# Kernel tuning notes

Measured on AMD Instinct MI355X. Metric: run time of the kernel, lower is better.

The kernel has to match this reference:

```python
import jax, jax.numpy as jnp
import numpy as np

GROUP_SIZE = 128
QMAX = 127.0  # int8 symmetric: 2^(8-1) - 1
EPS = 1e-8


def group_quant_dequant(t, group_size=GROUP_SIZE):
    """Group-wise symmetric int8 fake-quantize along the last dim.

    Groups of `group_size` along the last axis share one scale
    s = max|t| / 127; values are rounded/clipped to int8 range and
    immediately dequantized (q * s), which is the exact math of a
    group-quantized GEMM with inline dequantization.
    """
    shape = t.shape
    g = t.reshape(shape[:-1] + (shape[-1] // group_size, group_size))
    s = jnp.maximum(jnp.max(jnp.abs(g), axis=-1, keepdims=True) / QMAX, EPS)
    q = jnp.clip(jnp.round(g / s), -QMAX, QMAX)
    return (q * s).reshape(shape)


def setup_inputs() -> dict:
    key = jax.random.key(0)
    k0, k1, k2, k3 = jax.random.split(key, 4)
    B, S, H, I = 2, 2048, 4096, 11008
    x = jax.random.normal(k0, (B, S, H), dtype=jnp.float32)
    # Linear weights stored [out_features, in_features]; quant groups run
    # along the in_features (contraction) axis.
    w_gate = jax.random.normal(k1, (I, H), dtype=jnp.float32) * (1.0 / np.sqrt(H))
    w_up = jax.random.normal(k2, (I, H), dtype=jnp.float32) * (1.0 / np.sqrt(H))
    w_down = jax.random.normal(k3, (H, I), dtype=jnp.float32) * (1.0 / np.sqrt(I))
    return {"x": x, "w_gate": w_gate, "w_up": w_up, "w_down": w_down}


def reference(x, w_gate, w_up, w_down):
    # quantize input activations (QuantTensor(x))
    xq = group_quant_dequant(x)
    # gate/up quant-GEMMs with inline weight dequant
    gate = jnp.einsum('bsh,ih->bsi', xq, group_quant_dequant(w_gate))
    up = jnp.einsum('bsh,ih->bsi', xq, group_quant_dequant(w_up))
    # SwiGLU: SiLU(gate) * up, then requantize the hidden activation
    hidden = jax.nn.silu(gate) * up
    hq = group_quant_dequant(hidden)
    # down quant-GEMM -> dequantized float output
    out = jnp.einsum('bsi,hi->bsh', hq, group_quant_dequant(w_down))
    return out
```

## Files before the change

kernel.cpp:

```cpp
#include <hip/hip_runtime.h>
#include <math.h>

typedef int i32x4 __attribute__((ext_vector_type(4)));
typedef float f32x4 __attribute__((ext_vector_type(4)));
typedef float f32x2 __attribute__((ext_vector_type(2)));

#define QMAXF 127.0f
#define EPSQ 1e-8f

__device__ __forceinline__ void gl_lds16(const void* g, void* l) {
  __builtin_amdgcn_global_load_lds(
      (const __attribute__((address_space(1))) unsigned int*)g,
      (__attribute__((address_space(3))) unsigned int*)l, 16, 0, 0);
}
__device__ __forceinline__ void gl_lds4(const void* g, void* l) {
  __builtin_amdgcn_global_load_lds(
      (const __attribute__((address_space(1))) unsigned int*)g,
      (__attribute__((address_space(3))) unsigned int*)l, 4, 0, 0);
}

__global__ __launch_bounds__(256)
void qdq8(const float* __restrict__ in, char* __restrict__ q,
          float* __restrict__ sT, long n_groups, int gpr, int R) {
  long wid = (long)blockIdx.x * 4 + (threadIdx.x >> 6);
  if (wid >= n_groups) return;
  int lane = threadIdx.x & 63;
  long base = wid * 128 + lane * 2;
  f32x2 v = *(const f32x2*)(in + base);
  float m = fmaxf(fabsf(v.x), fabsf(v.y));
#pragma unroll
  for (int off = 32; off; off >>= 1) m = fmaxf(m, __shfl_xor(m, off));
  float s = fmaxf(m / QMAXF, EPSQ);
  int q0 = (int)fminf(fmaxf(rintf(v.x / s), -QMAXF), QMAXF);
  int q1 = (int)fminf(fmaxf(rintf(v.y / s), -QMAXF), QMAXF);
  *(unsigned short*)(q + base) =
      (unsigned short)((q0 & 0xff) | ((q1 & 0xff) << 8));
  if (lane == 0) {
    long row = wid / gpr;
    long gc = wid - row * gpr;
    sT[gc * (long)R + row] = s;
  }
}


__global__ __launch_bounds__(256) __attribute__((amdgpu_waves_per_eu(2, 2)))
void gemm_gu_i8(const char* __restrict__ Aq, const char* __restrict__ Bg,
                const char* __restrict__ Bu,
                const float* __restrict__ sAT, const float* __restrict__ sGT,
                const float* __restrict__ sUT,
                char* __restrict__ Hq, float* __restrict__ sHT,
                int M, int N, int K, int NBN) {
  __shared__ char sA[16384];
  __shared__ char sBG[16384];
  __shared__ char sBU[16384];
  __shared__ float sSa[128], sSg[128], sSu[128];
  __shared__ float rmx[2][128];
  __shared__ float rs[128];

  const int tid = threadIdx.x;
  const int lane = tid & 63;
  const int wid = tid >> 6;
  const int wr = (wid >> 1) * 64;
  const int wc = (wid & 1) * 64;
  const int l15 = lane & 15, l16 = lane >> 4;

  const int nwg = gridDim.x;
  const int wg = ((int)blockIdx.x & 7) * (nwg >> 3) + ((int)blockIdx.x >> 3);
  const long m0 = (long)(wg / NBN) * 128;
  const long n0 = (long)(wg % NBN) * 128;

  const char* gA[4];
  const char* gG[4];
  const char* gU[4];
#pragma unroll
  for (int k = 0; k < 4; k++) {
    int c = tid + 256 * k;
    long row = c >> 3;
    int off = ((c & 7) * 16) ^ ((int)(row & 7) << 4);
    gA[k] = Aq + (m0 + row) * K + off;
    gG[k] = Bg + (n0 + row) * K + off;
    gU[k] = Bu + (n0 + row) * K + off;
  }

  const int rdSwz = (l15 & 7) << 4;
  const int colK0 = (l16 * 16) ^ rdSwz;
  const int colK1 = (64 + l16 * 16) ^ rdSwz;

  f32x4 accg[4][4], accu[4][4];
#pragma unroll
  for (int i = 0; i < 4; i++)
#pragma unroll
    for (int j = 0; j < 4; j++) {
      accg[i][j] = (f32x4){0.f, 0.f, 0.f, 0.f};
      accu[i][j] = (f32x4){0.f, 0.f, 0.f, 0.f};
    }
  const i32x4 iz = {0, 0, 0, 0};

  const int KG = K >> 7;
  for (int g = 0; g < KG; ++g) {
    const long kb = (long)g << 7;
#pragma unroll
    for (int k = 0; k < 4; k++) {
      gl_lds16(gA[k] + kb, &sA[(tid + 256 * k) * 16]);
      gl_lds16(gG[k] + kb, &sBG[(tid + 256 * k) * 16]);
      gl_lds16(gU[k] + kb, &sBU[(tid + 256 * k) * 16]);
    }
    if (wid < 2) {
      gl_lds4(sAT + (long)g * M + m0 + tid, &sSa[wid * 64]);
      gl_lds4(sUT + (long)g * N + n0 + tid, &sSu[wid * 64]);
    } else {
      gl_lds4(sGT + (long)g * N + n0 + (tid - 128), &sSg[(wid - 2) * 64]);
    }
    __syncthreads();

    i32x4 af[4][2];
#pragma unroll
    for (int i = 0; i < 4; i++) {
      const int rb = (wr + i * 16 + l15) * 128;
      af[i][0] = *(const i32x4*)&sA[rb + colK0];
      af[i][1] = *(const i32x4*)&sA[rb + colK1];
    }
    f32x4 sa4[4];
#pragma unroll
    for (int i = 0; i < 4; i++)
      sa4[i] = *(const f32x4*)&sSa[wr + i * 16 + l16 * 4];

#pragma unroll
    for (int j = 0; j < 4; j++) {
      const int rbB = (wc + j * 16 + l15) * 128;
      i32x4 bgf[2], buf_[2];
      bgf[0] = *(const i32x4*)&sBG[rbB + colK0];
      bgf[1] = *(const i32x4*)&sBG[rbB + colK1];
      buf_[0] = *(const i32x4*)&sBU[rbB + colK0];
      buf_[1] = *(const i32x4*)&sBU[rbB + colK1];
      float sbg = sSg[wc + j * 16 + l15];
      float sbu = sSu[wc + j * 16 + l15];
#pragma unroll
      for (int i = 0; i < 4; i++) {
        i32x4 tg = __builtin_amdgcn_mfma_i32_16x16x64_i8(af[i][0], bgf[0], iz, 0, 0, 0);
        tg = __builtin_amdgcn_mfma_i32_16x16x64_i8(af[i][1], bgf[1], tg, 0, 0, 0);
        i32x4 tu = __builtin_amdgcn_mfma_i32_16x16x64_i8(af[i][0], buf_[0], iz, 0, 0, 0);
        tu = __builtin_amdgcn_mfma_i32_16x16x64_i8(af[i][1], buf_[1], tu, 0, 0, 0);
        f32x4 mg = sa4[i] * sbg;
        f32x4 mu = sa4[i] * sbu;
        accg[i][j] += mg * __builtin_convertvector(tg, f32x4);
        accu[i][j] += mu * __builtin_convertvector(tu, f32x4);
      }
    }
    __syncthreads();
  }

  float pm[4][4];
#pragma unroll
  for (int i = 0; i < 4; i++)
#pragma unroll
    for (int r = 0; r < 4; r++) pm[i][r] = 0.f;
#pragma unroll
  for (int i = 0; i < 4; i++)
#pragma unroll
    for (int j = 0; j < 4; j++)
#pragma unroll
      for (int r = 0; r < 4; r++) {
        float gv = accg[i][j][r];
        float h = gv / (1.f + expf(-gv)) * accu[i][j][r];
        accu[i][j][r] = h;
        pm[i][r] = fmaxf(pm[i][r], fabsf(h));
      }
#pragma unroll
  for (int i = 0; i < 4; i++)
#pragma unroll
    for (int r = 0; r < 4; r++) {
      pm[i][r] = fmaxf(pm[i][r], __shfl_xor(pm[i][r], 1));
      pm[i][r] = fmaxf(pm[i][r], __shfl_xor(pm[i][r], 2));
      pm[i][r] = fmaxf(pm[i][r], __shfl_xor(pm[i][r], 4));
      pm[i][r] = fmaxf(pm[i][r], __shfl_xor(pm[i][r], 8));
    }
#pragma unroll
  for (int i = 0; i < 4; i++)
#pragma unroll
    for (int r = 0; r < 4; r++)
      if (l15 == i * 4 + r) rmx[wid & 1][wr + i * 16 + l16 * 4 + r] = pm[i][r];
  __syncthreads();
  if (tid < 128) {
    float mx = fmaxf(rmx[0][tid], rmx[1][tid]);
    float s = fmaxf(mx / QMAXF, EPSQ);
    rs[tid] = s;
    sHT[(n0 >> 7) * (long)M + m0 + tid] = s;
  }
  __syncthreads();
#pragma unroll
  for (int i = 0; i < 4; i++) {
    f32x4 sr = *(const f32x4*)&rs[wr + i * 16 + l16 * 4];
#pragma unroll
    for (int j = 0; j < 4; j++)
#pragma unroll
      for (int r = 0; r < 4; r++) {
        float qv = fminf(fmaxf(rintf(accu[i][j][r] / sr[r]), -QMAXF), QMAXF);
        sA[(wr + i * 16 + l16 * 4 + r) * 128 + wc + j * 16 + l15] = (char)(int)qv;
      }
  }
  __syncthreads();
  {
    int row = tid >> 1, seg = tid & 1;
    const i32x4* src = (const i32x4*)&sA[row * 128 + seg * 64];
    i32x4* dst = (i32x4*)(Hq + (m0 + row) * N + n0 + seg * 64);
#pragma unroll
    for (int k = 0; k < 4; k++) dst[k] = src[k];
  }
}

__global__ __launch_bounds__(256) __attribute__((amdgpu_waves_per_eu(2, 2)))
void gemm_dn_i8(const char* __restrict__ Aq, const char* __restrict__ Bq,
                const float* __restrict__ sAT, const float* __restrict__ sBT,
                float* __restrict__ C, int M, int N, int K, int NBN) {
  __shared__ char sA[16384];
  __shared__ char sB[16384];
  __shared__ float sSa[128], sSb[128];

  const int tid = threadIdx.x;
  const int lane = tid & 63;
  const int wid = tid >> 6;
  const int wr = (wid >> 1) * 64;
  const int wc = (wid & 1) * 64;
  const int l15 = lane & 15, l16 = lane >> 4;

  const int nwg = gridDim.x;
  const int wg = ((int)blockIdx.x & 7) * (nwg >> 3) + ((int)blockIdx.x >> 3);
  const long m0 = (long)(wg / NBN) * 128;
  const long n0 = (long)(wg % NBN) * 128;

  const char* gA[4];
  const char* gB[4];
#pragma unroll
  for (int k = 0; k < 4; k++) {
    int c = tid + 256 * k;
    long row = c >> 3;
    int off = ((c & 7) * 16) ^ ((int)(row & 7) << 4);
    gA[k] = Aq + (m0 + row) * K + off;
    gB[k] = Bq + (n0 + row) * K + off;
  }

  const int rdSwz = (l15 & 7) << 4;
  const int colK0 = (l16 * 16) ^ rdSwz;
  const int colK1 = (64 + l16 * 16) ^ rdSwz;

  f32x4 acc[4][4];
#pragma unroll
  for (int i = 0; i < 4; i++)
#pragma unroll
    for (int j = 0; j < 4; j++) acc[i][j] = (f32x4){0.f, 0.f, 0.f, 0.f};
  const i32x4 iz = {0, 0, 0, 0};

  const int KG = K >> 7;
  for (int g = 0; g < KG; ++g) {
    const long kb = (long)g << 7;
#pragma unroll
    for (int k = 0; k < 4; k++) {
      gl_lds16(gA[k] + kb, &sA[(tid + 256 * k) * 16]);
      gl_lds16(gB[k] + kb, &sB[(tid + 256 * k) * 16]);
    }
    if (wid < 2) {
      gl_lds4(sAT + (long)g * M + m0 + tid, &sSa[wid * 64]);
    } else {
      gl_lds4(sBT + (long)g * N + n0 + (tid - 128), &sSb[(wid - 2) * 64]);
    }
    __syncthreads();

    i32x4 af[4][2];
#pragma unroll
    for (int i = 0; i < 4; i++) {
      const int rb = (wr + i * 16 + l15) * 128;
      af[i][0] = *(const i32x4*)&sA[rb + colK0];
      af[i][1] = *(const i32x4*)&sA[rb + colK1];
    }
    f32x4 sa4[4];
#pragma unroll
    for (int i = 0; i < 4; i++)
      sa4[i] = *(const f32x4*)&sSa[wr + i * 16 + l16 * 4];

#pragma unroll
    for (int j = 0; j < 4; j++) {
      const int rbB = (wc + j * 16 + l15) * 128;
      i32x4 bf[2];
      bf[0] = *(const i32x4*)&sB[rbB + colK0];
      bf[1] = *(const i32x4*)&sB[rbB + colK1];
      float sb = sSb[wc + j * 16 + l15];
#pragma unroll
      for (int i = 0; i < 4; i++) {
        i32x4 t = __builtin_amdgcn_mfma_i32_16x16x64_i8(af[i][0], bf[0], iz, 0, 0, 0);
        t = __builtin_amdgcn_mfma_i32_16x16x64_i8(af[i][1], bf[1], t, 0, 0, 0);
        f32x4 ms = sa4[i] * sb;
        acc[i][j] += ms * __builtin_convertvector(t, f32x4);
      }
    }
    __syncthreads();
  }

#pragma unroll
  for (int i = 0; i < 4; i++)
#pragma unroll
    for (int j = 0; j < 4; j++)
#pragma unroll
      for (int r = 0; r < 4; r++) {
        long row = m0 + wr + i * 16 + l16 * 4 + r;
        long col = n0 + wc + j * 16 + l15;
        C[row * N + col] = acc[i][j][r];
      }
}

extern "C" void kernel_launch(void* const* d_in, const int* in_sizes, int n_in,
                              void* d_out, int out_size, void* d_ws, size_t ws_size,
                              hipStream_t stream) {
  (void)n_in; (void)out_size;
  const float* x  = (const float*)d_in[0];
  const float* wg = (const float*)d_in[1];
  const float* wu = (const float*)d_in[2];
  const float* wd = (const float*)d_in[3];
  float* out = (float*)d_out;

  const long H = 4096;
  const long M = in_sizes[0] / H;
  const long I = in_sizes[1] / H;
  const long GH = H >> 7;
  const long GI = I >> 7;

  char* ws = (char*)d_ws;
  size_t off = 0;
  char* xq  = ws + off; off += (size_t)(M * H);
  char* wgq = ws + off; off += (size_t)(I * H);
  char* wuq = ws + off; off += (size_t)(I * H);
  char* wdq = ws + off; off += (size_t)(H * I);
  char* hq  = ws + off; off += (size_t)(M * I);
  float* s_x = (float*)(ws + off); off += (size_t)(GH * M) * 4;
  float* s_g = (float*)(ws + off); off += (size_t)(GH * I) * 4;
  float* s_u = (float*)(ws + off); off += (size_t)(GH * I) * 4;
  float* s_d = (float*)(ws + off); off += (size_t)(GI * H) * 4;
  float* s_h = (float*)(ws + off); off += (size_t)(GI * M) * 4;
  if (ws_size < off) return;

  {
    long ng;
    ng = M * H / 128;
    qdq8<<<dim3((unsigned)((ng + 3) / 4)), dim3(256), 0, stream>>>(x, xq, s_x, ng, (int)GH, (int)M);
    ng = I * H / 128;
    qdq8<<<dim3((unsigned)((ng + 3) / 4)), dim3(256), 0, stream>>>(wg, wgq, s_g, ng, (int)GH, (int)I);
    qdq8<<<dim3((unsigned)((ng + 3) / 4)), dim3(256), 0, stream>>>(wu, wuq, s_u, ng, (int)GH, (int)I);
    ng = H * I / 128;
    qdq8<<<dim3((unsigned)((ng + 3) / 4)), dim3(256), 0, stream>>>(wd, wdq, s_d, ng, (int)GI, (int)H);
  }

  {
    const int NBN = (int)GI;
    const int grid = (int)(M / 128) * NBN;
    gemm_gu_i8<<<dim3(grid), dim3(256), 0, stream>>>(
        xq, wgq, wuq, s_x, s_g, s_u, hq, s_h, (int)M, (int)I, (int)H, NBN);
  }
  {
    const int NBN = (int)GH;
    const int grid = (int)(M / 128) * NBN;
    gemm_dn_i8<<<dim3(grid), dim3(256), 0, stream>>>(
        hq, wdq, s_h, s_d, out, (int)M, (int)H, (int)I, NBN);
  }
}
```

Measured before the change: 1.168 ms.

## Double-buffer LDS and enlarge GEMM tiles to 256x128 with 512 threads

Both int8 GEMM kernels switch from static 48KB/32KB shared buffers to dynamic LDS holding two stages. The next K-group's operand and scale tiles are loaded asynchronously (global_load_lds) while the current group is computed, which removes one barrier per iteration. The block tile grows from 128x128 to 256x128 with 8 waves, which halves the grid and increases reuse of the B/weight tiles. The large LDS footprint (~135KB and ~99KB) likely limits each CU to one block. That trades occupancy-based latency hiding for explicit prefetching.

```diff
diff --git a/kernel.cpp b/kernel.cpp
--- a/kernel.cpp
+++ b/kernel.cpp
@@ -43,44 +43,37 @@
 }
 
 
-__global__ __launch_bounds__(256) __attribute__((amdgpu_waves_per_eu(2, 2)))
+#define GU_SC 131072
+#define GU_RMX 135168
+#define GU_RS 137216
+#define GU_LDS 138240
+
+__global__ __launch_bounds__(512, 2)
 void gemm_gu_i8(const char* __restrict__ Aq, const char* __restrict__ Bg,
                 const char* __restrict__ Bu,
                 const float* __restrict__ sAT, const float* __restrict__ sGT,
                 const float* __restrict__ sUT,
                 char* __restrict__ Hq, float* __restrict__ sHT,
                 int M, int N, int K, int NBN) {
-  __shared__ char sA[16384];
-  __shared__ char sBG[16384];
-  __shared__ char sBU[16384];
-  __shared__ float sSa[128], sSg[128], sSu[128];
-  __shared__ float rmx[2][128];
-  __shared__ float rs[128];
-
+  extern __shared__ __align__(16) char smem[];
   const int tid = threadIdx.x;
   const int lane = tid & 63;
   const int wid = tid >> 6;
-  const int wr = (wid >> 1) * 64;
-  const int wc = (wid & 1) * 64;
+  const int wm = wid >> 1, wn = wid & 1;
+  const int wr = wm * 64, wc = wn * 64;
   const int l15 = lane & 15, l16 = lane >> 4;
 
   const int nwg = gridDim.x;
   const int wg = ((int)blockIdx.x & 7) * (nwg >> 3) + ((int)blockIdx.x >> 3);
-  const long m0 = (long)(wg / NBN) * 128;
+  const long m0 = (long)(wg / NBN) * 256;
   const long n0 = (long)(wg % NBN) * 128;
 
-  const char* gA[4];
-  const char* gG[4];
-  const char* gU[4];
-#pragma unroll
-  for (int k = 0; k < 4; k++) {
-    int c = tid + 256 * k;
-    long row = c >> 3;
-    int off = ((c & 7) * 16) ^ ((int)(row & 7) << 4);
-    gA[k] = Aq + (m0 + row) * K + off;
-    gG[k] = Bg + (n0 + row) * K + off;
-    gU[k] = Bu + (n0 + row) * K + off;
-  }
+  const long rowS = tid >> 3;
+  const int offS = ((tid & 7) * 16) ^ ((int)(rowS & 7) << 4);
+  const long kstr = 64L * K;
+  const char* gA0 = Aq + (m0 + rowS) * K + offS;
+  const char* gG0 = Bg + (n0 + rowS) * K + offS;
+  const char* gU0 = Bu + (n0 + rowS) * K + offS;
 
   const int rdSwz = (l15 & 7) << 4;
   const int colK0 = (l16 * 16) ^ rdSwz;
@@ -95,46 +88,60 @@
       accu[i][j] = (f32x4){0.f, 0.f, 0.f, 0.f};
     }
   const i32x4 iz = {0, 0, 0, 0};
-
   const int KG = K >> 7;
+
+#define GU_STAGE(gg, bb)                                                      \
+  {                                                                           \
+    const long kb = (long)(gg) << 7;                                          \
+    char* tb = smem + (bb) * 65536;                                           \
+    _Pragma("unroll") for (int k = 0; k < 4; k++)                             \
+        gl_lds16(gA0 + kb + k * kstr, tb + (tid + 512 * k) * 16);             \
+    _Pragma("unroll") for (int k = 0; k < 2; k++) {                           \
+      gl_lds16(gG0 + kb + k * kstr, tb + 32768 + (tid + 512 * k) * 16);       \
+      gl_lds16(gU0 + kb + k * kstr, tb + 49152 + (tid + 512 * k) * 16);       \
+    }                                                                         \
+    char* sc = smem + GU_SC + (bb) * 2048;                                    \
+    if (wid < 4) {                                                            \
+      gl_lds4(sAT + (long)(gg) * M + m0 + tid, sc + wid * 256);               \
+    } else if (wid < 6) {                                                     \
+      gl_lds4(sGT + (long)(gg) * N + n0 + (tid - 256), sc + 1024 + (wid - 4) * 256); \
+    } else {                                                                  \
+      gl_lds4(sUT + (long)(gg) * N + n0 + (tid - 384), sc + 1536 + (wid - 6) * 256); \
+    }                                                                         \
+  }
+
+  GU_STAGE(0, 0);
+  __syncthreads();
+
   for (int g = 0; g < KG; ++g) {
-    const long kb = (long)g << 7;
-#pragma unroll
-    for (int k = 0; k < 4; k++) {
-      gl_lds16(gA[k] + kb, &sA[(tid + 256 * k) * 16]);
-      gl_lds16(gG[k] + kb, &sBG[(tid + 256 * k) * 16]);
-      gl_lds16(gU[k] + kb, &sBU[(tid + 256 * k) * 16]);
-    }
-    if (wid < 2) {
-      gl_lds4(sAT + (long)g * M + m0 + tid, &sSa[wid * 64]);
-      gl_lds4(sUT + (long)g * N + n0 + tid, &sSu[wid * 64]);
-    } else {
-      gl_lds4(sGT + (long)g * N + n0 + (tid - 128), &sSg[(wid - 2) * 64]);
-    }
-    __syncthreads();
+    const int cb = g & 1;
+    if (g + 1 < KG) GU_STAGE(g + 1, cb ^ 1);
+
+    const char* tb = smem + cb * 65536;
+    const float* sc = (const float*)(smem + GU_SC + cb * 2048);
 
     i32x4 af[4][2];
 #pragma unroll
     for (int i = 0; i < 4; i++) {
       const int rb = (wr + i * 16 + l15) * 128;
-      af[i][0] = *(const i32x4*)&sA[rb + colK0];
-      af[i][1] = *(const i32x4*)&sA[rb + colK1];
+      af[i][0] = *(const i32x4*)(tb + rb + colK0);
+      af[i][1] = *(const i32x4*)(tb + rb + colK1);
     }
     f32x4 sa4[4];
 #pragma unroll
     for (int i = 0; i < 4; i++)
-      sa4[i] = *(const f32x4*)&sSa[wr + i * 16 + l16 * 4];
+      sa4[i] = *(const f32x4*)(sc + wr + i * 16 + l16 * 4);
 
 #pragma unroll
     for (int j = 0; j < 4; j++) {
       const int rbB = (wc + j * 16 + l15) * 128;
       i32x4 bgf[2], buf_[2];
-      bgf[0] = *(const i32x4*)&sBG[rbB + colK0];
-      bgf[1] = *(const i32x4*)&sBG[rbB + colK1];
-      buf_[0] = *(const i32x4*)&sBU[rbB + colK0];
-      buf_[1] = *(const i32x4*)&sBU[rbB + colK1];
-      float sbg = sSg[wc + j * 16 + l15];
-      float sbu = sSu[wc + j * 16 + l15];
+      bgf[0] = *(const i32x4*)(tb + 32768 + rbB + colK0);
+      bgf[1] = *(const i32x4*)(tb + 32768 + rbB + colK1);
+      buf_[0] = *(const i32x4*)(tb + 49152 + rbB + colK0);
+      buf_[1] = *(const i32x4*)(tb + 49152 + rbB + colK1);
+      float sbg = sc[256 + wc + j * 16 + l15];
+      float sbu = sc[384 + wc + j * 16 + l15];
 #pragma unroll
       for (int i = 0; i < 4; i++) {
         i32x4 tg = __builtin_amdgcn_mfma_i32_16x16x64_i8(af[i][0], bgf[0], iz, 0, 0, 0);
@@ -150,6 +157,8 @@
     __syncthreads();
   }
 
+  float* rmx = (float*)(smem + GU_RMX);
+  float* rs = (float*)(smem + GU_RS);
   float pm[4][4];
 #pragma unroll
   for (int i = 0; i < 4; i++)
@@ -179,66 +188,62 @@
   for (int i = 0; i < 4; i++)
 #pragma unroll
     for (int r = 0; r < 4; r++)
-      if (l15 == i * 4 + r) rmx[wid & 1][wr + i * 16 + l16 * 4 + r] = pm[i][r];
-  __syncthreads();
-  if (tid < 128) {
-    float mx = fmaxf(rmx[0][tid], rmx[1][tid]);
+      if (l15 == i * 4 + r) rmx[wn * 256 + wr + i * 16 + l16 * 4 + r] = pm[i][r];
+  __syncthreads();
+  if (tid < 256) {
+    float mx = fmaxf(rmx[tid], rmx[256 + tid]);
     float s = fmaxf(mx / QMAXF, EPSQ);
     rs[tid] = s;
     sHT[(n0 >> 7) * (long)M + m0 + tid] = s;
   }
   __syncthreads();
+  char* sQ = smem;
 #pragma unroll
   for (int i = 0; i < 4; i++) {
-    f32x4 sr = *(const f32x4*)&rs[wr + i * 16 + l16 * 4];
+    f32x4 sr = *(const f32x4*)(rs + wr + i * 16 + l16 * 4);
 #pragma unroll
     for (int j = 0; j < 4; j++)
 #pragma unroll
       for (int r = 0; r < 4; r++) {
         float qv = fminf(fmaxf(rintf(accu[i][j][r] / sr[r]), -QMAXF), QMAXF);
-        sA[(wr + i * 16 + l16 * 4 + r) * 128 + wc + j * 16 + l15] = (char)(int)qv;
+        sQ[(wr + i * 16 + l16 * 4 + r) * 128 + wc + j * 16 + l15] = (char)(int)qv;
       }
   }
   __syncthreads();
   {
     int row = tid >> 1, seg = tid & 1;
-    const i32x4* src = (const i32x4*)&sA[row * 128 + seg * 64];
+    const i32x4* src = (const i32x4*)(sQ + row * 128 + seg * 64);
     i32x4* dst = (i32x4*)(Hq + (m0 + row) * N + n0 + seg * 64);
 #pragma unroll
     for (int k = 0; k < 4; k++) dst[k] = src[k];
   }
 }
 
-__global__ __launch_bounds__(256) __attribute__((amdgpu_waves_per_eu(2, 2)))
+#define DN_SC 98304
+#define DN_LDS 101376
+
+__global__ __launch_bounds__(512, 2)
 void gemm_dn_i8(const char* __restrict__ Aq, const char* __restrict__ Bq,
                 const float* __restrict__ sAT, const float* __restrict__ sBT,
                 float* __restrict__ C, int M, int N, int K, int NBN) {
-  __shared__ char sA[16384];
-  __shared__ char sB[16384];
-  __shared__ float sSa[128], sSb[128];
-
+  extern __shared__ __align__(16) char smem[];
   const int tid = threadIdx.x;
   const int lane = tid & 63;
   const int wid = tid >> 6;
-  const int wr = (wid >> 1) * 64;
-  const int wc = (wid & 1) * 64;
+  const int wm = wid >> 1, wn = wid & 1;
+  const int wr = wm * 64, wc = wn * 64;
   const int l15 = lane & 15, l16 = lane >> 4;
 
   const int nwg = gridDim.x;
   const int wg = ((int)blockIdx.x & 7) * (nwg >> 3) + ((int)blockIdx.x >> 3);
-  const long m0 = (long)(wg / NBN) * 128;
+  const long m0 = (long)(wg / NBN) * 256;
   const long n0 = (long)(wg % NBN) * 128;
 
-  const char* gA[4];
-  const char* gB[4];
-#pragma unroll
-  for (int k = 0; k < 4; k++) {
-    int c = tid + 256 * k;
-    long row = c >> 3;
-    int off = ((c & 7) * 16) ^ ((int)(row & 7) << 4);
-    gA[k] = Aq + (m0 + row) * K + off;
-    gB[k] = Bq + (n0 + row) * K + off;
-  }
+  const long rowS = tid >> 3;
+  const int offS = ((tid & 7) * 16) ^ ((int)(rowS & 7) << 4);
+  const long kstr = 64L * K;
+  const char* gA0 = Aq + (m0 + rowS) * K + offS;
+  const char* gB0 = Bq + (n0 + rowS) * K + offS;
 
   const int rdSwz = (l15 & 7) << 4;
   const int colK0 = (l16 * 16) ^ rdSwz;
@@ -250,41 +255,53 @@
 #pragma unroll
     for (int j = 0; j < 4; j++) acc[i][j] = (f32x4){0.f, 0.f, 0.f, 0.f};
   const i32x4 iz = {0, 0, 0, 0};
-
   const int KG = K >> 7;
+
+#define DN_STAGE(gg, bb)                                                      \
+  {                                                                           \
+    const long kb = (long)(gg) << 7;                                          \
+    char* tb = smem + (bb) * 49152;                                           \
+    _Pragma("unroll") for (int k = 0; k < 4; k++)                             \
+        gl_lds16(gA0 + kb + k * kstr, tb + (tid + 512 * k) * 16);             \
+    _Pragma("unroll") for (int k = 0; k < 2; k++)                             \
+        gl_lds16(gB0 + kb + k * kstr, tb + 32768 + (tid + 512 * k) * 16);     \
+    char* sc = smem + DN_SC + (bb) * 1536;                                    \
+    if (wid < 4) {                                                            \
+      gl_lds4(sAT + (long)(gg) * M + m0 + tid, sc + wid * 256);               \
+    } else if (wid < 6) {                                                     \
+      gl_lds4(sBT + (long)(gg) * N + n0 + (tid - 256), sc + 1024 + (wid - 4) * 256); \
+    }                                                                         \
+  }
+
+  DN_STAGE(0, 0);
+  __syncthreads();
+
   for (int g = 0; g < KG; ++g) {
-    const long kb = (long)g << 7;
-#pragma unroll
-    for (int k = 0; k < 4; k++) {
-      gl_lds16(gA[k] + kb, &sA[(tid + 256 * k) * 16]);
-      gl_lds16(gB[k] + kb, &sB[(tid + 256 * k) * 16]);
-    }
-    if (wid < 2) {
-      gl_lds4(sAT + (long)g * M + m0 + tid, &sSa[wid * 64]);
-    } else {
-      gl_lds4(sBT + (long)g * N + n0 + (tid - 128), &sSb[(wid - 2) * 64]);
-    }
-    __syncthreads();
+    const int cb = g & 1;
+    if (g + 1 < KG) DN_STAGE(g + 1, cb ^ 1);
+
+    const char* tb = smem + cb * 49152;
+    const float* sc = (const float*)(smem + DN_SC + cb * 1536);
 
     i32x4 af[4][2];
 #pragma unroll
     for (int i = 0; i < 4; i++) {
       const int rb = (wr + i * 16 + l15) * 128;
-      af[i][0] = *(const i32x4*)&sA[rb + colK0];
-      af[i][1] = *(const i32x4*)&sA[rb + colK1];
+      af[i][0] = *(const i32x4*)(tb + rb + colK0);
+      af[i][1] = *(const i32x4*)(tb + rb + colK1);
     }
     f32x4 sa4[4];
 #pragma unroll
     for (int i = 0; i < 4; i++)
-      sa4[i] = *(const f32x4*)&sSa[wr + i * 16 + l16 * 4];
+      sa4[i] = *(const f32x4*)(sc + wr + i * 16 + l16 * 4);
 
 #pragma unroll
     for (int j = 0; j < 4; j++) {
       const int rbB = (wc + j * 16 + l15) * 128;
       i32x4 bf[2];
-      bf[0] = *(const i32x4*)&sB[rbB + colK0];
-      bf[1] = *(const i32x4*)&sB[rbB + colK1];
-      float sb = sSb[wc + j * 16 + l15];
+      bf[0] = *(const i32x4*)(tb + 32768 + rbB + colK0);
+      bf[1] = *(const i32x4*)(tb + 32768 + rbB + colK1);
+      float sb = sc[256 + wc + j * 16 + l15];
 #pragma unroll
       for (int i = 0; i < 4; i++) {
         i32x4 t = __builtin_amdgcn_mfma_i32_16x16x64_i8(af[i][0], bf[0], iz, 0, 0, 0);
@@ -338,6 +355,11 @@
   float* s_h = (float*)(ws + off); off += (size_t)(GI * M) * 4;
   if (ws_size < off) return;
 
+  hipFuncSetAttribute((const void*)gemm_gu_i8,
+                      hipFuncAttributeMaxDynamicSharedMemorySize, GU_LDS);
+  hipFuncSetAttribute((const void*)gemm_dn_i8,
+                      hipFuncAttributeMaxDynamicSharedMemorySize, DN_LDS);
+
   {
     long ng;
     ng = M * H / 128;
@@ -351,14 +373,14 @@
 
   {
     const int NBN = (int)GI;
-    const int grid = (int)(M / 128) * NBN;
-    gemm_gu_i8<<<dim3(grid), dim3(256), 0, stream>>>(
+    const int grid = (int)(M / 256) * NBN;
+    gemm_gu_i8<<<dim3(grid), dim3(512), GU_LDS, stream>>>(
         xq, wgq, wuq, s_x, s_g, s_u, hq, s_h, (int)M, (int)I, (int)H, NBN);
   }
   {
     const int NBN = (int)GH;
-    const int grid = (int)(M / 128) * NBN;
-    gemm_dn_i8<<<dim3(grid), dim3(256), 0, stream>>>(
+    const int grid = (int)(M / 256) * NBN;
+    gemm_dn_i8<<<dim3(grid), dim3(512), DN_LDS, stream>>>(
         hq, wdq, s_h, s_d, out, (int)M, (int)H, (int)I, NBN);
   }
 }
```

Result: faster. 1.117 ms (-4.4%).

## Shrink GEMM tiles to 64x128 with 512-thread blocks and 8 waves

Applied to the files above, without the earlier changes.

Both int8 GEMM kernels move from 128x128 tiles with 4 waves (64x64 per wave) to 64x128 tiles with 8 waves (32x32 per wave) and 512 threads per block. The launch grid doubles. This raises wave count and occupancy and lowers register pressure per wave. In exchange, each MFMA gets less operand reuse and global traffic per output rises, because the B tile is reloaded twice as often across M.

```diff
diff --git a/kernel.cpp b/kernel.cpp
--- a/kernel.cpp
+++ b/kernel.cpp
@@ -43,90 +43,83 @@
 }
 
 
-__global__ __launch_bounds__(256) __attribute__((amdgpu_waves_per_eu(2, 2)))
+__global__ __launch_bounds__(512, 4)
 void gemm_gu_i8(const char* __restrict__ Aq, const char* __restrict__ Bg,
                 const char* __restrict__ Bu,
                 const float* __restrict__ sAT, const float* __restrict__ sGT,
                 const float* __restrict__ sUT,
                 char* __restrict__ Hq, float* __restrict__ sHT,
                 int M, int N, int K, int NBN) {
-  __shared__ char sA[16384];
-  __shared__ char sBG[16384];
-  __shared__ char sBU[16384];
-  __shared__ float sSa[128], sSg[128], sSu[128];
-  __shared__ float rmx[2][128];
-  __shared__ float rs[128];
+  __shared__ __align__(16) char sA[8192];
+  __shared__ __align__(16) char sBG[16384];
+  __shared__ __align__(16) char sBU[16384];
+  __shared__ float sSa[64], sSg[128], sSu[128];
+  __shared__ float rmx[4][64];
+  __shared__ float rs[64];
 
   const int tid = threadIdx.x;
   const int lane = tid & 63;
   const int wid = tid >> 6;
-  const int wr = (wid >> 1) * 64;
-  const int wc = (wid & 1) * 64;
+  const int wm = wid >> 2, wn = wid & 3;
+  const int wr = wm * 32, wc = wn * 32;
   const int l15 = lane & 15, l16 = lane >> 4;
 
   const int nwg = gridDim.x;
   const int wg = ((int)blockIdx.x & 7) * (nwg >> 3) + ((int)blockIdx.x >> 3);
-  const long m0 = (long)(wg / NBN) * 128;
+  const long m0 = (long)(wg / NBN) * 64;
   const long n0 = (long)(wg % NBN) * 128;
 
-  const char* gA[4];
-  const char* gG[4];
-  const char* gU[4];
-#pragma unroll
-  for (int k = 0; k < 4; k++) {
-    int c = tid + 256 * k;
-    long row = c >> 3;
-    int off = ((c & 7) * 16) ^ ((int)(row & 7) << 4);
-    gA[k] = Aq + (m0 + row) * K + off;
-    gG[k] = Bg + (n0 + row) * K + off;
-    gU[k] = Bu + (n0 + row) * K + off;
-  }
+  const long rowS = tid >> 3;
+  const int offS = ((tid & 7) * 16) ^ ((int)(rowS & 7) << 4);
+  const long kstr = 64L * K;
+  const char* gA0 = Aq + (m0 + rowS) * K + offS;
+  const char* gG0 = Bg + (n0 + rowS) * K + offS;
+  const char* gU0 = Bu + (n0 + rowS) * K + offS;
 
   const int rdSwz = (l15 & 7) << 4;
   const int colK0 = (l16 * 16) ^ rdSwz;
   const int colK1 = (64 + l16 * 16) ^ rdSwz;
 
-  f32x4 accg[4][4], accu[4][4];
-#pragma unroll
-  for (int i = 0; i < 4; i++)
-#pragma unroll
-    for (int j = 0; j < 4; j++) {
+  f32x4 accg[2][2], accu[2][2];
+#pragma unroll
+  for (int i = 0; i < 2; i++)
+#pragma unroll
+    for (int j = 0; j < 2; j++) {
       accg[i][j] = (f32x4){0.f, 0.f, 0.f, 0.f};
       accu[i][j] = (f32x4){0.f, 0.f, 0.f, 0.f};
     }
   const i32x4 iz = {0, 0, 0, 0};
-
   const int KG = K >> 7;
+
   for (int g = 0; g < KG; ++g) {
     const long kb = (long)g << 7;
-#pragma unroll
-    for (int k = 0; k < 4; k++) {
-      gl_lds16(gA[k] + kb, &sA[(tid + 256 * k) * 16]);
-      gl_lds16(gG[k] + kb, &sBG[(tid + 256 * k) * 16]);
-      gl_lds16(gU[k] + kb, &sBU[(tid + 256 * k) * 16]);
-    }
-    if (wid < 2) {
-      gl_lds4(sAT + (long)g * M + m0 + tid, &sSa[wid * 64]);
-      gl_lds4(sUT + (long)g * N + n0 + tid, &sSu[wid * 64]);
-    } else {
-      gl_lds4(sGT + (long)g * N + n0 + (tid - 128), &sSg[(wid - 2) * 64]);
-    }
+    gl_lds16(gA0 + kb, &sA[tid * 16]);
+#pragma unroll
+    for (int k = 0; k < 2; k++) {
+      gl_lds16(gG0 + kb + k * kstr, &sBG[(tid + 512 * k) * 16]);
+      gl_lds16(gU0 + kb + k * kstr, &sBU[(tid + 512 * k) * 16]);
+    }
+    if (wid == 0) gl_lds4(sAT + (long)g * M + m0 + lane, &sSa[0]);
+    else if (wid == 1) gl_lds4(sGT + (long)g * N + n0 + lane, &sSg[0]);
+    else if (wid == 2) gl_lds4(sGT + (long)g * N + n0 + 64 + lane, &sSg[64]);
+    else if (wid == 3) gl_lds4(sUT + (long)g * N + n0 + lane, &sSu[0]);
+    else if (wid == 4) gl_lds4(sUT + (long)g * N + n0 + 64 + lane, &sSu[64]);
     __syncthreads();
 
-    i32x4 af[4][2];
-#pragma unroll
-    for (int i = 0; i < 4; i++) {
+    i32x4 af[2][2];
+#pragma unroll
+    for (int i = 0; i < 2; i++) {
       const int rb = (wr + i * 16 + l15) * 128;
       af[i][0] = *(const i32x4*)&sA[rb + colK0];
       af[i][1] = *(const i32x4*)&sA[rb + colK1];
     }
-    f32x4 sa4[4];
-#pragma unroll
-    for (int i = 0; i < 4; i++)
+    f32x4 sa4[2];
+#pragma unroll
+    for (int i = 0; i < 2; i++)
       sa4[i] = *(const f32x4*)&sSa[wr + i * 16 + l16 * 4];
 
 #pragma unroll
-    for (int j = 0; j < 4; j++) {
+    for (int j = 0; j < 2; j++) {
       const int rbB = (wc + j * 16 + l15) * 128;
       i32x4 bgf[2], buf_[2];
       bgf[0] = *(const i32x4*)&sBG[rbB + colK0];
@@ -136,29 +129,27 @@
       float sbg = sSg[wc + j * 16 + l15];
       float sbu = sSu[wc + j * 16 + l15];
 #pragma unroll
-      for (int i = 0; i < 4; i++) {
+      for (int i = 0; i < 2; i++) {
         i32x4 tg = __builtin_amdgcn_mfma_i32_16x16x64_i8(af[i][0], bgf[0], iz, 0, 0, 0);
         tg = __builtin_amdgcn_mfma_i32_16x16x64_i8(af[i][1], bgf[1], tg, 0, 0, 0);
         i32x4 tu = __builtin_amdgcn_mfma_i32_16x16x64_i8(af[i][0], buf_[0], iz, 0, 0, 0);
         tu = __builtin_amdgcn_mfma_i32_16x16x64_i8(af[i][1], buf_[1], tu, 0, 0, 0);
-        f32x4 mg = sa4[i] * sbg;
-        f32x4 mu = sa4[i] * sbu;
-        accg[i][j] += mg * __builtin_convertvector(tg, f32x4);
-        accu[i][j] += mu * __builtin_convertvector(tu, f32x4);
+        accg[i][j] += (sa4[i] * sbg) * __builtin_convertvector(tg, f32x4);
+        accu[i][j] += (sa4[i] * sbu) * __builtin_convertvector(tu, f32x4);
       }
     }
     __syncthreads();
   }
 
-  float pm[4][4];
-#pragma unroll
-  for (int i = 0; i < 4; i++)
+  float pm[2][4];
+#pragma unroll
+  for (int i = 0; i < 2; i++)
 #pragma unroll
     for (int r = 0; r < 4; r++) pm[i][r] = 0.f;
 #pragma unroll
-  for (int i = 0; i < 4; i++)
-#pragma unroll
-    for (int j = 0; j < 4; j++)
+  for (int i = 0; i < 2; i++)
+#pragma unroll
+    for (int j = 0; j < 2; j++)
 #pragma unroll
       for (int r = 0; r < 4; r++) {
         float gv = accg[i][j][r];
@@ -167,7 +158,7 @@
         pm[i][r] = fmaxf(pm[i][r], fabsf(h));
       }
 #pragma unroll
-  for (int i = 0; i < 4; i++)
+  for (int i = 0; i < 2; i++)
 #pragma unroll
     for (int r = 0; r < 4; r++) {
       pm[i][r] = fmaxf(pm[i][r], __shfl_xor(pm[i][r], 1));
@@ -176,23 +167,24 @@
       pm[i][r] = fmaxf(pm[i][r], __shfl_xor(pm[i][r], 8));
     }
 #pragma unroll
-  for (int i = 0; i < 4; i++)
+  for (int i = 0; i < 2; i++)
 #pragma unroll
     for (int r = 0; r < 4; r++)
-      if (l15 == i * 4 + r) rmx[wid & 1][wr + i * 16 + l16 * 4 + r] = pm[i][r];
+      if (l15 == i * 4 + r) rmx[wn][wr + i * 16 + l16 * 4 + r] = pm[i][r];
   __syncthreads();
-  if (tid < 128) {
-    float mx = fmaxf(rmx[0][tid], rmx[1][tid]);
+  if (tid < 64) {
+    float mx = fmaxf(fmaxf(rmx[0][tid], rmx[1][tid]),
+                     fmaxf(rmx[2][tid], rmx[3][tid]));
     float s = fmaxf(mx / QMAXF, EPSQ);
     rs[tid] = s;
     sHT[(n0 >> 7) * (long)M + m0 + tid] = s;
   }
   __syncthreads();
 #pragma unroll
-  for (int i = 0; i < 4; i++) {
+  for (int i = 0; i < 2; i++) {
     f32x4 sr = *(const f32x4*)&rs[wr + i * 16 + l16 * 4];
 #pragma unroll
-    for (int j = 0; j < 4; j++)
+    for (int j = 0; j < 2; j++)
 #pragma unroll
       for (int r = 0; r < 4; r++) {
         float qv = fminf(fmaxf(rintf(accu[i][j][r] / sr[r]), -QMAXF), QMAXF);
@@ -201,105 +193,94 @@
   }
   __syncthreads();
   {
-    int row = tid >> 1, seg = tid & 1;
-    const i32x4* src = (const i32x4*)&sA[row * 128 + seg * 64];
-    i32x4* dst = (i32x4*)(Hq + (m0 + row) * N + n0 + seg * 64);
-#pragma unroll
-    for (int k = 0; k < 4; k++) dst[k] = src[k];
-  }
-}
-
-__global__ __launch_bounds__(256) __attribute__((amdgpu_waves_per_eu(2, 2)))
+    long row = tid >> 3;
+    int off = (tid & 7) * 16;
+    *(i32x4*)(Hq + (m0 + row) * N + n0 + off) = *(const i32x4*)&sA[row * 128 + off];
+  }
+}
+
+__global__ __launch_bounds__(512, 4)
 void gemm_dn_i8(const char* __restrict__ Aq, const char* __restrict__ Bq,
                 const float* __restrict__ sAT, const float* __restrict__ sBT,
                 float* __restrict__ C, int M, int N, int K, int NBN) {
-  __shared__ char sA[16384];
-  __shared__ char sB[16384];
-  __shared__ float sSa[128], sSb[128];
+  __shared__ __align__(16) char sA[8192];
+  __shared__ __align__(16) char sB[16384];
+  __shared__ float sSa[64], sSb[128];
 
   const int tid = threadIdx.x;
   const int lane = tid & 63;
   const int wid = tid >> 6;
-  const int wr = (wid >> 1) * 64;
-  const int wc = (wid & 1) * 64;
+  const int wm = wid >> 2, wn = wid & 3;
+  const int wr = wm * 32, wc = wn * 32;
   const int l15 = lane & 15, l16 = lane >> 4;
 
   const int nwg = gridDim.x;
   const int wg = ((int)blockIdx.x & 7) * (nwg >> 3) + ((int)blockIdx.x >> 3);
-  const long m0 = (long)(wg / NBN) * 128;
+  const long m0 = (long)(wg / NBN) * 64;
   const long n0 = (long)(wg % NBN) * 128;
 
-  const char* gA[4];
-  const char* gB[4];
-#pragma unroll
-  for (int k = 0; k < 4; k++) {
-    int c = tid + 256 * k;
-    long row = c >> 3;
-    int off = ((c & 7) * 16) ^ ((int)(row & 7) << 4);
-    gA[k] = Aq + (m0 + row) * K + off;
-    gB[k] = Bq + (n0 + row) * K + off;
-  }
+  const long rowS = tid >> 3;
+  const int offS = ((tid & 7) * 16) ^ ((int)(rowS & 7) << 4);
+  const long kstr = 64L * K;
+  const char* gA0 = Aq + (m0 + rowS) * K + offS;
+  const char* gB0 = Bq + (n0 + rowS) * K + offS;
 
   const int rdSwz = (l15 & 7) << 4;
   const int colK0 = (l16 * 16) ^ rdSwz;
   const int colK1 = (64 + l16 * 16) ^ rdSwz;
 
-  f32x4 acc[4][4];
-#pragma unroll
-  for (int i = 0; i < 4; i++)
-#pragma unroll
-    for (int j = 0; j < 4; j++) acc[i][j] = (f32x4){0.f, 0.f, 0.f, 0.f};
+  f32x4 acc[2][2];
+#pragma unroll
+  for (int i = 0; i < 2; i++)
+#pragma unroll
+    for (int j = 0; j < 2; j++) acc[i][j] = (f32x4){0.f, 0.f, 0.f, 0.f};
   const i32x4 iz = {0, 0, 0, 0};
-
   const int KG = K >> 7;
+
   for (int g = 0; g < KG; ++g) {
     const long kb = (long)g << 7;
-#pragma unroll
-    for (int k = 0; k < 4; k++) {
-      gl_lds16(gA[k] + kb, &sA[(tid + 256 * k) * 16]);
-      gl_lds16(gB[k] + kb, &sB[(tid + 256 * k) * 16]);
-    }
-    if (wid < 2) {
-      gl_lds4(sAT + (long)g * M + m0 + tid, &sSa[wid * 64]);
-    } else {
-      gl_lds4(sBT + (long)g * N + n0 + (tid - 128), &sSb[(wid - 2) * 64]);
-    }
+    gl_lds16(gA0 + kb, &sA[tid * 16]);
+#pragma unroll
+    for (int k = 0; k < 2; k++)
+      gl_lds16(gB0 + kb + k * kstr, &sB[(tid + 512 * k) * 16]);
+    if (wid == 0) gl_lds4(sAT + (long)g * M + m0 + lane, &sSa[0]);
+    else if (wid == 1) gl_lds4(sBT + (long)g * N + n0 + lane, &sSb[0]);
+    else if (wid == 2) gl_lds4(sBT + (long)g * N + n0 + 64 + lane, &sSb[64]);
     __syncthreads();
 
-    i32x4 af[4][2];
-#pragma unroll
-    for (int i = 0; i < 4; i++) {
+    i32x4 af[2][2];
+#pragma unroll
+    for (int i = 0; i < 2; i++) {
       const int rb = (wr + i * 16 + l15) * 128;
       af[i][0] = *(const i32x4*)&sA[rb + colK0];
       af[i][1] = *(const i32x4*)&sA[rb + colK1];
     }
-    f32x4 sa4[4];
-#pragma unroll
-    for (int i = 0; i < 4; i++)
+    f32x4 sa4[2];
+#pragma unroll
+    for (int i = 0; i < 2; i++)
       sa4[i] = *(const f32x4*)&sSa[wr + i * 16 + l16 * 4];
 
 #pragma unroll
-    for (int j = 0; j < 4; j++) {
+    for (int j = 0; j < 2; j++) {
       const int rbB = (wc + j * 16 + l15) * 128;
       i32x4 bf[2];
       bf[0] = *(const i32x4*)&sB[rbB + colK0];
       bf[1] = *(const i32x4*)&sB[rbB + colK1];
       float sb = sSb[wc + j * 16 + l15];
 #pragma unroll
-      for (int i = 0; i < 4; i++) {
+      for (int i = 0; i < 2; i++) {
         i32x4 t = __builtin_amdgcn_mfma_i32_16x16x64_i8(af[i][0], bf[0], iz, 0, 0, 0);
         t = __builtin_amdgcn_mfma_i32_16x16x64_i8(af[i][1], bf[1], t, 0, 0, 0);
-        f32x4 ms = sa4[i] * sb;
-        acc[i][j] += ms * __builtin_convertvector(t, f32x4);
+        acc[i][j] += (sa4[i] * sb) * __builtin_convertvector(t, f32x4);
       }
     }
     __syncthreads();
   }
 
 #pragma unroll
-  for (int i = 0; i < 4; i++)
-#pragma unroll
-    for (int j = 0; j < 4; j++)
+  for (int i = 0; i < 2; i++)
+#pragma unroll
+    for (int j = 0; j < 2; j++)
 #pragma unroll
       for (int r = 0; r < 4; r++) {
         long row = m0 + wr + i * 16 + l16 * 4 + r;
@@ -351,14 +332,14 @@
 
   {
     const int NBN = (int)GI;
-    const int grid = (int)(M / 128) * NBN;
-    gemm_gu_i8<<<dim3(grid), dim3(256), 0, stream>>>(
+    const int grid = (int)(M / 64) * NBN;
+    gemm_gu_i8<<<dim3(grid), dim3(512), 0, stream>>>(
         xq, wgq, wuq, s_x, s_g, s_u, hq, s_h, (int)M, (int)I, (int)H, NBN);
   }
   {
     const int NBN = (int)GH;
-    const int grid = (int)(M / 128) * NBN;
-    gemm_dn_i8<<<dim3(grid), dim3(256), 0, stream>>>(
+    const int grid = (int)(M / 64) * NBN;
+    gemm_dn_i8<<<dim3(grid), dim3(512), 0, stream>>>(
         hq, wdq, s_h, s_d, out, (int)M, (int)H, (int)I, NBN);
   }
 }
```

New measurement: 1.494 ms. 27.9% more time.
